# Kernel tuning notes

Measured on AMD Instinct MI355X. Metric: run time of the kernel, lower is better.

## Reference

```python
import jax, jax.numpy as jnp
import numpy as np

B, S, R, H, NH, HD = 32, 1026, 256, 1024, 16, 64

def setup_inputs() -> dict:
    key = jax.random.key(0)
    ks = jax.random.split(key, 8)
    sc = 0.02
    return {
        "q_low": jax.random.normal(ks[0], (B, S, R), jnp.float32),
        "k_low": jax.random.normal(ks[1], (B, S, R), jnp.float32),
        "v_low": jax.random.normal(ks[2], (B, S, R), jnp.float32),
        "Wq": jax.random.normal(ks[3], (R, H), jnp.float32) * sc,
        "bq": jnp.zeros((H,), jnp.float32),
        "Wk": jax.random.normal(ks[4], (R, H), jnp.float32) * sc,
        "bk": jnp.zeros((H,), jnp.float32),
        "Wv": jax.random.normal(ks[5], (R, H), jnp.float32) * sc,
        "bv": jnp.zeros((H,), jnp.float32),
        "Wo_down": jax.random.normal(ks[6], (H, R), jnp.float32) * sc,
    }

def reference(q_low, k_low, v_low, Wq, bq, Wk, bk, Wv, bv, Wo_down):
    # Up-project low-rank activations to full Q, K, V: [B,S,R] @ [R,H] -> [B,S,H]
    q = q_low @ Wq + bq
    k = k_low @ Wk + bk
    v = v_low @ Wv + bv
    # split heads: [B,S,NH,HD] -> [B,NH,S,HD]
    def split(x):
        return x.reshape(B, S, NH, HD).transpose(0, 2, 1, 3)
    qh, kh, vh = split(q), split(k), split(v)
    scores = jnp.einsum('bhqd,bhkd->bhqk', qh, kh) / jnp.sqrt(jnp.float32(HD))
    probs = jax.nn.softmax(scores, axis=-1)  # dropout p=0
    ctx = jnp.einsum('bhqk,bhkd->bhqd', probs, vh)
    ctx = ctx.transpose(0, 2, 1, 3).reshape(B, S, H)
    # Down-project with low-rank activation (gelu)
    out_low = jax.nn.gelu(ctx @ Wo_down, approximate=False)
    return out_low
```

## Files before the change

kernel.cpp:

```cpp
#include <hip/hip_runtime.h>
#include <hip/hip_bf16.h>
#include <math.h>

using short8   = __attribute__((ext_vector_type(8))) short;
using floatx4  = __attribute__((ext_vector_type(4))) float;
using floatx16 = __attribute__((ext_vector_type(16))) float;

#define B_N  32
#define S_N  1026
#define R_N  256
#define H_N  1024
#define NH_N 16
#define HD_N 64
#define SP_N 1088
#define KTILES 17

__device__ __forceinline__ float bf2f(__hip_bfloat16 x) { return __bfloat162float(x); }
__device__ __forceinline__ __hip_bfloat16 f2bf(float x) { return __float2bfloat16(x); }

__device__ __forceinline__ float fast_exp2(float x) {
#if __has_builtin(__builtin_amdgcn_exp2f)
    return __builtin_amdgcn_exp2f(x);
#else
    return exp2f(x);
#endif
}

__device__ __forceinline__ unsigned cvtpk(float lo, float hi_) {
    unsigned r;
    asm("v_cvt_pk_bf16_f32 %0, %1, %2" : "=v"(r) : "v"(lo), "v"(hi_));
    return r;
}

__device__ __forceinline__ void gl_lds16(const void* g, void* l) {
    __builtin_amdgcn_global_load_lds(
        (const __attribute__((address_space(1))) unsigned int*)g,
        (__attribute__((address_space(3))) unsigned int*)l, 16, 0, 0);
}

__device__ __forceinline__ short8 cvt8(const float* __restrict__ p) {
    floatx4 a = *(const floatx4*)p;
    floatx4 b = *(const floatx4*)(p + 4);
    short8 o;
    __hip_bfloat16* op = (__hip_bfloat16*)&o;
    op[0] = f2bf(a[0]); op[1] = f2bf(a[1]); op[2] = f2bf(a[2]); op[3] = f2bf(a[3]);
    op[4] = f2bf(b[0]); op[5] = f2bf(b[1]); op[6] = f2bf(b[2]); op[7] = f2bf(b[3]);
    return o;
}

__global__ __launch_bounds__(256) void transpose3_kernel(
    const float* __restrict__ a, const float* __restrict__ b, const float* __restrict__ c,
    __hip_bfloat16* __restrict__ oa, __hip_bfloat16* __restrict__ ob,
    __hip_bfloat16* __restrict__ oc, int K, int N) {
    __shared__ __hip_bfloat16 t[32][33];
    const float* in = (blockIdx.z == 0) ? a : (blockIdx.z == 1) ? b : c;
    __hip_bfloat16* out = (blockIdx.z == 0) ? oa : (blockIdx.z == 1) ? ob : oc;
    const int k0 = blockIdx.x * 32, n0 = blockIdx.y * 32;
    const int tx = threadIdx.x & 31, ty = threadIdx.x >> 5;
#pragma unroll
    for (int j = 0; j < 32; j += 8)
        t[ty + j][tx] = f2bf(in[(size_t)(k0 + ty + j) * N + n0 + tx]);
    __syncthreads();
#pragma unroll
    for (int j = 0; j < 32; j += 8)
        out[(size_t)(n0 + ty + j) * K + k0 + tx] = t[tx][ty + j];
}

__global__ __launch_bounds__(256) void transpose_kernel(const float* __restrict__ in,
                                                        __hip_bfloat16* __restrict__ out,
                                                        int K, int N) {
    __shared__ __hip_bfloat16 t[32][33];
    const int k0 = blockIdx.x * 32, n0 = blockIdx.y * 32;
    const int tx = threadIdx.x & 31, ty = threadIdx.x >> 5;
#pragma unroll
    for (int j = 0; j < 32; j += 8)
        t[ty + j][tx] = f2bf(in[(size_t)(k0 + ty + j) * N + n0 + tx]);
    __syncthreads();
#pragma unroll
    for (int j = 0; j < 32; j += 8)
        out[(size_t)(n0 + ty + j) * K + k0 + tx] = t[tx][ty + j];
}

__global__ __launch_bounds__(256) void cvtx_kernel(
    const float* __restrict__ q, const float* __restrict__ k, const float* __restrict__ v,
    __hip_bfloat16* __restrict__ oq, __hip_bfloat16* __restrict__ ok,
    __hip_bfloat16* __restrict__ ov, int n8) {
    int idx = blockIdx.x * 256 + threadIdx.x;
    if (idx >= n8) return;
    const float* s = (blockIdx.y == 0) ? q : (blockIdx.y == 1) ? k : v;
    __hip_bfloat16* d = (blockIdx.y == 0) ? oq : (blockIdx.y == 1) ? ok : ov;
    *(short8*)(d + (size_t)idx * 8) = cvt8(s + (size_t)idx * 8);
}

__global__ void padv_kernel(__hip_bfloat16* __restrict__ Vt, int total) {
    int idx = blockIdx.x * 256 + threadIdx.x;
    if (idx < total) {
        int p  = idx % (SP_N - S_N);
        int rd = idx / (SP_N - S_N);
        Vt[(size_t)rd * SP_N + S_N + p] = f2bf(0.f);
    }
}

__global__ __launch_bounds__(256) void qkvproj_kernel(
    const __hip_bfloat16* __restrict__ Xq, const __hip_bfloat16* __restrict__ Xk,
    const __hip_bfloat16* __restrict__ Xv,
    const __hip_bfloat16* __restrict__ WqT, const __hip_bfloat16* __restrict__ WkT,
    const __hip_bfloat16* __restrict__ WvT,
    const float* __restrict__ bq, const float* __restrict__ bk,
    const float* __restrict__ bv,
    __hip_bfloat16* __restrict__ Qc, __hip_bfloat16* __restrict__ Kc,
    __hip_bfloat16* __restrict__ Vc, int Mc, float qscale) {
    __shared__ __hip_bfloat16 As[2][128][32];
    __shared__ __hip_bfloat16 Bs[2][128][32];
    const int z = blockIdx.z;
    const __hip_bfloat16* X  = (z == 0) ? Xq  : (z == 1) ? Xk  : Xv;
    const __hip_bfloat16* WT = (z == 0) ? WqT : (z == 1) ? WkT : WvT;
    const float* bias        = (z == 0) ? bq  : (z == 1) ? bk  : bv;
    __hip_bfloat16* out      = (z == 0) ? Qc  : (z == 1) ? Kc  : Vc;
    const float oscale = (z == 0) ? qscale : 1.0f;
    const int mode = (z == 2);

    const int tid  = threadIdx.x;
    const int wave = tid >> 6, lane = tid & 63;
    const int quad = lane >> 4, l16 = lane & 15;
    const int tm = blockIdx.x * 128, tn = blockIdx.y * 128;
    const int mw = (wave >> 1) * 64, nw = (wave & 1) * 64;
    const int lrow = lane >> 2, lchunk = lane & 3;

    floatx4 acc[4][4] = {};

    const int g0 = wave, g1 = wave + 4;
    int ra0 = tm + g0 * 16 + lrow; if (ra0 >= Mc) ra0 = Mc - 1;
    int ra1 = tm + g1 * 16 + lrow; if (ra1 >= Mc) ra1 = Mc - 1;
    const int rb0 = tn + g0 * 16 + lrow, rb1 = tn + g1 * 16 + lrow;

    auto stage = [&](int bb, int kk) {
        gl_lds16(X  + (size_t)ra0 * R_N + kk + lchunk * 8, &As[bb][g0 * 16][0]);
        gl_lds16(X  + (size_t)ra1 * R_N + kk + lchunk * 8, &As[bb][g1 * 16][0]);
        gl_lds16(WT + (size_t)rb0 * R_N + kk + lchunk * 8, &Bs[bb][g0 * 16][0]);
        gl_lds16(WT + (size_t)rb1 * R_N + kk + lchunk * 8, &Bs[bb][g1 * 16][0]);
    };

    stage(0, 0);
    __syncthreads();

    for (int t = 0; t < R_N / 32; ++t) {
        const int bb = t & 1;
        if (t + 1 < R_N / 32) stage(bb ^ 1, (t + 1) * 32);
        short8 af[4], bfr[4];
#pragma unroll
        for (int mb = 0; mb < 4; ++mb) af[mb]  = *(short8*)&As[bb][mw + mb * 16 + l16][quad * 8];
#pragma unroll
        for (int nb = 0; nb < 4; ++nb) bfr[nb] = *(short8*)&Bs[bb][nw + nb * 16 + l16][quad * 8];
        if (mode == 0) {
#pragma unroll
            for (int mb = 0; mb < 4; ++mb)
#pragma unroll
                for (int nb = 0; nb < 4; ++nb)
                    acc[mb][nb] = __builtin_amdgcn_mfma_f32_16x16x32_bf16(af[mb], bfr[nb], acc[mb][nb], 0, 0, 0);
        } else {
#pragma unroll
            for (int mb = 0; mb < 4; ++mb)
#pragma unroll
                for (int nb = 0; nb < 4; ++nb)
                    acc[mb][nb] = __builtin_amdgcn_mfma_f32_16x16x32_bf16(bfr[nb], af[mb], acc[mb][nb], 0, 0, 0);
        }
        __syncthreads();
    }

#pragma unroll
    for (int mb = 0; mb < 4; ++mb)
#pragma unroll
        for (int nb = 0; nb < 4; ++nb)
#pragma unroll
            for (int r = 0; r < 4; ++r) {
                int m, n;
                if (mode == 0) { m = tm + mw + mb * 16 + quad * 4 + r; n = tn + nw + nb * 16 + l16; }
                else           { n = tn + nw + nb * 16 + quad * 4 + r; m = tm + mw + mb * 16 + l16; }
                if (m >= Mc) continue;
                float v = oscale * (acc[mb][nb][r] + bias[n]);
                int bl = m / S_N, s = m - bl * S_N;
                int h = n >> 6, d = n & 63;
                size_t off = (mode == 0)
                    ? ((size_t)((bl * NH_N + h) * S_N + s)) * HD_N + d
                    : ((size_t)((bl * NH_N + h) * HD_N + d)) * SP_N + s;
                out[off] = f2bf(v);
            }
}

__global__ __launch_bounds__(256, 3) void attn_kernel(
    const __hip_bfloat16* __restrict__ Qh,
    const __hip_bfloat16* __restrict__ Kh,
    const __hip_bfloat16* __restrict__ Vt,
    __hip_bfloat16* __restrict__ ctx) {
    __shared__ __hip_bfloat16 Kl[2][64][64];
    __shared__ __hip_bfloat16 Vl[2][64][64];

    const int bh  = blockIdx.x;
    const int q0  = blockIdx.y * 128;
    const int tid = threadIdx.x;
    const int wave = tid >> 6, lane = tid & 63;
    const int c = lane & 31, hi = lane >> 5, c7 = c & 7;
    const size_t base  = (size_t)bh * S_N * HD_N;
    const size_t vbase = (size_t)bh * HD_N * SP_N;

    const int lr = lane >> 3;
    const int sc = (lane & 7) ^ lr;

    short8 qf[4];
    {
        int qrow = q0 + wave * 32 + c;
        if (qrow > S_N - 1) qrow = S_N - 1;
        const __hip_bfloat16* qp = Qh + base + (size_t)qrow * HD_N + hi * 8;
#pragma unroll
        for (int i = 0; i < 4; ++i) qf[i] = *(const short8*)(qp + 16 * i);
    }

    floatx16 oacc[2] = {};
    float lsum = 0.f;

    auto stage = [&](int bb, int kt) {
#pragma unroll
        for (int j = 0; j < 2; ++j) {
            int r = 16 * wave + 8 * j + lr;
            int krow = kt + r;
            if (krow > S_N - 1) krow = S_N - 1;
            gl_lds16(Kh + base + (size_t)krow * HD_N + sc * 8,
                     &Kl[bb][16 * wave + 8 * j][0]);
            gl_lds16(Vt + vbase + (size_t)r * SP_N + kt + sc * 8,
                     &Vl[bb][16 * wave + 8 * j][0]);
        }
    };

    stage(0, 0);
    __syncthreads();

    int bb = 0;
    for (int t = 0; t < KTILES; ++t) {
        const int kt = t * 64;
        if (t + 1 < KTILES) stage(bb ^ 1, kt + 64);
        const bool last = (kt + 64 > S_N);

        short8 pa[2][2];
#pragma unroll
        for (int sub = 0; sub < 2; ++sub) {
            floatx16 sacc = {};
            __builtin_amdgcn_s_setprio(1);
#pragma unroll
            for (int i = 0; i < 4; ++i) {
                short8 kf = *(const short8*)&Kl[bb][32 * sub + c][(((2 * i + hi) ^ c7) << 3)];
                sacc = __builtin_amdgcn_mfma_f32_32x32x16_bf16(kf, qf[i], sacc, 0, 0, 0);
            }
            __builtin_amdgcn_s_setprio(0);
            float ps[16];
            if (!last) {
#pragma unroll
                for (int r = 0; r < 16; ++r) ps[r] = fast_exp2(sacc[r]);
            } else {
#pragma unroll
                for (int r = 0; r < 16; ++r) {
                    int key = kt + 32 * sub + (r & 3) + 8 * (r >> 2) + 4 * hi;
                    ps[r] = (key < S_N) ? fast_exp2(sacc[r]) : 0.f;
                }
            }
#pragma unroll
            for (int r = 0; r < 16; ++r) lsum += ps[r];
#pragma unroll
            for (int step = 0; step < 2; ++step) {
                unsigned w0 = cvtpk(ps[8 * step + 0], ps[8 * step + 1]);
                unsigned w1 = cvtpk(ps[8 * step + 2], ps[8 * step + 3]);
                unsigned w2 = cvtpk(ps[8 * step + 4], ps[8 * step + 5]);
                unsigned w3 = cvtpk(ps[8 * step + 6], ps[8 * step + 7]);
                asm("v_permlane32_swap_b32 %0, %1" : "+v"(w0), "+v"(w2));
                asm("v_permlane32_swap_b32 %0, %1" : "+v"(w1), "+v"(w3));
                union { unsigned u[4]; short8 s; } fu;
                fu.u[0] = w0; fu.u[1] = w1; fu.u[2] = w2; fu.u[3] = w3;
                pa[sub][step] = fu.s;
            }
        }

        __builtin_amdgcn_s_setprio(1);
#pragma unroll
        for (int db = 0; db < 2; ++db)
#pragma unroll
            for (int sub = 0; sub < 2; ++sub)
#pragma unroll
                for (int step = 0; step < 2; ++step) {
                    short8 vf = *(const short8*)
                        &Vl[bb][32 * db + c][((((sub * 2 + step) * 2 + hi) ^ c7) << 3)];
                    oacc[db] = __builtin_amdgcn_mfma_f32_32x32x16_bf16(pa[sub][step], vf, oacc[db], 0, 0, 0);
                }
        __builtin_amdgcn_s_setprio(0);

        __syncthreads();
        bb ^= 1;
    }

    lsum += __shfl_xor(lsum, 32);
    float rs = 1.0f / lsum;

    const int bl = bh / NH_N, h = bh - bl * NH_N;
    const int srow0 = q0 + wave * 32;
#pragma unroll
    for (int r = 0; r < 16; ++r) {
        int q = (r & 3) + 8 * (r >> 2) + 4 * hi;
        float rr = __shfl(rs, q, 32);
        int s = srow0 + q;
        if (s < S_N) {
            size_t o = ((size_t)(bl * S_N + s)) * H_N + h * HD_N + c;
            ctx[o]      = f2bf(oacc[0][r] * rr);
            ctx[o + 32] = f2bf(oacc[1][r] * rr);
        }
    }
}

__global__ __launch_bounds__(256) void dproj_kernel(
    const __hip_bfloat16* __restrict__ X,
    const __hip_bfloat16* __restrict__ WT,
    float* __restrict__ out,
    int Mc) {
    __shared__ __hip_bfloat16 As[2][128][32];
    __shared__ __hip_bfloat16 Bs[2][128][32];
    const int tid  = threadIdx.x;
    const int wave = tid >> 6, lane = tid & 63;
    const int quad = lane >> 4, l16 = lane & 15;
    const int tm = blockIdx.x * 128, tn = blockIdx.y * 128;
    const int mw = (wave >> 1) * 64, nw = (wave & 1) * 64;
    const int lrow = lane >> 2, lchunk = lane & 3;

    floatx4 acc[4][4] = {};

    const int g0 = wave, g1 = wave + 4;
    int ra0 = tm + g0 * 16 + lrow; if (ra0 >= Mc) ra0 = Mc - 1;
    int ra1 = tm + g1 * 16 + lrow; if (ra1 >= Mc) ra1 = Mc - 1;
    const int rb0 = tn + g0 * 16 + lrow, rb1 = tn + g1 * 16 + lrow;

    auto stage = [&](int bb, int kk) {
        gl_lds16(X  + (size_t)ra0 * H_N + kk + lchunk * 8, &As[bb][g0 * 16][0]);
        gl_lds16(X  + (size_t)ra1 * H_N + kk + lchunk * 8, &As[bb][g1 * 16][0]);
        gl_lds16(WT + (size_t)rb0 * H_N + kk + lchunk * 8, &Bs[bb][g0 * 16][0]);
        gl_lds16(WT + (size_t)rb1 * H_N + kk + lchunk * 8, &Bs[bb][g1 * 16][0]);
    };

    stage(0, 0);
    __syncthreads();

    for (int t = 0; t < H_N / 32; ++t) {
        const int bb = t & 1;
        if (t + 1 < H_N / 32) stage(bb ^ 1, (t + 1) * 32);
        short8 af[4], bfr[4];
#pragma unroll
        for (int mb = 0; mb < 4; ++mb) af[mb]  = *(short8*)&As[bb][mw + mb * 16 + l16][quad * 8];
#pragma unroll
        for (int nb = 0; nb < 4; ++nb) bfr[nb] = *(short8*)&Bs[bb][nw + nb * 16 + l16][quad * 8];
#pragma unroll
        for (int mb = 0; mb < 4; ++mb)
#pragma unroll
            for (int nb = 0; nb < 4; ++nb)
                acc[mb][nb] = __builtin_amdgcn_mfma_f32_16x16x32_bf16(af[mb], bfr[nb], acc[mb][nb], 0, 0, 0);
        __syncthreads();
    }

#pragma unroll
    for (int mb = 0; mb < 4; ++mb)
#pragma unroll
        for (int nb = 0; nb < 4; ++nb)
#pragma unroll
            for (int r = 0; r < 4; ++r) {
                int m = tm + mw + mb * 16 + quad * 4 + r;
                int n = tn + nw + nb * 16 + l16;
                if (m >= Mc) continue;
                float x = acc[mb][nb][r];
                float g = 0.5f * x * (1.0f + erff(x * 0.70710678118654752f));
                out[(size_t)m * R_N + n] = g;
            }
}

extern "C" void kernel_launch(void* const* d_in, const int* in_sizes, int n_in,
                              void* d_out, int out_size, void* d_ws, size_t ws_size,
                              hipStream_t stream) {
    const float* q_low = (const float*)d_in[0];
    const float* k_low = (const float*)d_in[1];
    const float* v_low = (const float*)d_in[2];
    const float* Wq    = (const float*)d_in[3];
    const float* bq    = (const float*)d_in[4];
    const float* Wk    = (const float*)d_in[5];
    const float* bk    = (const float*)d_in[6];
    const float* Wv    = (const float*)d_in[7];
    const float* bv    = (const float*)d_in[8];
    const float* Wo    = (const float*)d_in[9];
    float* out = (float*)d_out;
    (void)in_sizes; (void)n_in; (void)out_size;

    const float QSCALE = 0.125f * 1.44269504088896f;
    const size_t SZ_W = (size_t)H_N * R_N * 2;

    int C = 32;
    while (C > 1) {
        size_t qk = (size_t)C * NH_N * S_N * HD_N * 2;
        size_t vv = (size_t)C * NH_N * HD_N * SP_N * 2;
        size_t cx = (size_t)C * S_N * H_N * 2;
        if (4 * SZ_W + 2 * qk + vv + cx <= ws_size) break;
        C >>= 1;
    }

    char* ws = (char*)d_ws;
    const size_t SZ_QK = (size_t)C * NH_N * S_N * HD_N * 2;
    const size_t SZ_V  = (size_t)C * NH_N * HD_N * SP_N * 2;
    __hip_bfloat16* WqT = (__hip_bfloat16*)(ws);
    __hip_bfloat16* WkT = (__hip_bfloat16*)(ws + SZ_W);
    __hip_bfloat16* WvT = (__hip_bfloat16*)(ws + 2 * SZ_W);
    __hip_bfloat16* WoT = (__hip_bfloat16*)(ws + 3 * SZ_W);
    __hip_bfloat16* Qc  = (__hip_bfloat16*)(ws + 4 * SZ_W);
    __hip_bfloat16* Kc  = (__hip_bfloat16*)(ws + 4 * SZ_W + SZ_QK);
    __hip_bfloat16* Vc  = (__hip_bfloat16*)(ws + 4 * SZ_W + 2 * SZ_QK);
    __hip_bfloat16* ctc = (__hip_bfloat16*)(ws + 4 * SZ_W + 2 * SZ_QK + SZ_V);

    {
        dim3 tg(R_N / 32, H_N / 32, 3);
        transpose3_kernel<<<tg, 256, 0, stream>>>(Wq, Wk, Wv, WqT, WkT, WvT, R_N, H_N);
        dim3 to(H_N / 32, R_N / 32);
        transpose_kernel<<<to, 256, 0, stream>>>(Wo, WoT, H_N, R_N);
    }

    {
        int total = C * NH_N * HD_N * (SP_N - S_N);
        padv_kernel<<<(total + 255) / 256, 256, 0, stream>>>(Vc, total);
    }

    for (int c0 = 0; c0 < B_N; c0 += C) {
        const int Mc = C * S_N;
        const size_t xoff = (size_t)c0 * S_N * R_N;

        __hip_bfloat16* Xq = ctc;
        __hip_bfloat16* Xk = ctc + (size_t)Mc * R_N;
        __hip_bfloat16* Xv = ctc + 2 * (size_t)Mc * R_N;
        {
            int n8 = Mc * R_N / 8;
            dim3 cg((n8 + 255) / 256, 3);
            cvtx_kernel<<<cg, 256, 0, stream>>>(q_low + xoff, k_low + xoff, v_low + xoff,
                                                Xq, Xk, Xv, n8);
        }

        dim3 pg((Mc + 127) / 128, H_N / 128, 3);
        qkvproj_kernel<<<pg, 256, 0, stream>>>(Xq, Xk, Xv, WqT, WkT, WvT,
                                               bq, bk, bv, Qc, Kc, Vc, Mc, QSCALE);

        dim3 ag(C * NH_N, (S_N + 127) / 128);
        attn_kernel<<<ag, 256, 0, stream>>>(Qc, Kc, Vc, ctc);

        dim3 dg((Mc + 127) / 128, R_N / 128);
        dproj_kernel<<<dg, 256, 0, stream>>>(ctc, WoT, out + xoff, Mc);
    }
}
```

Measured before the change: 643.4 us.

## Widen GEMM K-tiles with swizzled LDS, XCD-remap blocks, shrink dproj M-tile

```diff
diff --git a/kernel.cpp b/kernel.cpp
--- a/kernel.cpp
+++ b/kernel.cpp
@@ -36,6 +36,10 @@
     __builtin_amdgcn_global_load_lds(
         (const __attribute__((address_space(1))) unsigned int*)g,
         (__attribute__((address_space(3))) unsigned int*)l, 16, 0, 0);
+}
+
+__device__ __forceinline__ int xcd_swz(int o, int nwg) {
+    return ((nwg & 7) == 0) ? ((o & 7) * (nwg >> 3) + (o >> 3)) : o;
 }
 
 __device__ __forceinline__ short8 cvt8(const float* __restrict__ p) {
@@ -110,60 +114,83 @@
     const float* __restrict__ bv,
     __hip_bfloat16* __restrict__ Qc, __hip_bfloat16* __restrict__ Kc,
     __hip_bfloat16* __restrict__ Vc, int Mc, float qscale) {
-    __shared__ __hip_bfloat16 As[2][128][32];
-    __shared__ __hip_bfloat16 Bs[2][128][32];
-    const int z = blockIdx.z;
-    const __hip_bfloat16* X  = (z == 0) ? Xq  : (z == 1) ? Xk  : Xv;
-    const __hip_bfloat16* WT = (z == 0) ? WqT : (z == 1) ? WkT : WvT;
-    const float* bias        = (z == 0) ? bq  : (z == 1) ? bk  : bv;
-    __hip_bfloat16* out      = (z == 0) ? Qc  : (z == 1) ? Kc  : Vc;
-    const float oscale = (z == 0) ? qscale : 1.0f;
-    const int mode = (z == 2);
+    __shared__ __hip_bfloat16 As[2][128][64];
+    __shared__ __hip_bfloat16 Bs[2][128][64];
+
+    const int nx = gridDim.x;
+    const int nwg = nx * 8 * 3;
+    const int o = blockIdx.x + nx * (blockIdx.y + 8 * blockIdx.z);
+    const int tlin = xcd_swz(o, nwg);
+    const int ty = tlin & 7;
+    const int rest = tlin >> 3;
+    const int tx = rest % nx, tz = rest / nx;
+
+    const __hip_bfloat16* X  = (tz == 0) ? Xq  : (tz == 1) ? Xk  : Xv;
+    const __hip_bfloat16* WT = (tz == 0) ? WqT : (tz == 1) ? WkT : WvT;
+    const float* bias        = (tz == 0) ? bq  : (tz == 1) ? bk  : bv;
+    __hip_bfloat16* out      = (tz == 0) ? Qc  : (tz == 1) ? Kc  : Vc;
+    const float oscale = (tz == 0) ? qscale : 1.0f;
+    const int mode = (tz == 2);
 
     const int tid  = threadIdx.x;
     const int wave = tid >> 6, lane = tid & 63;
     const int quad = lane >> 4, l16 = lane & 15;
-    const int tm = blockIdx.x * 128, tn = blockIdx.y * 128;
+    const int tm = tx * 128, tn = ty * 128;
     const int mw = (wave >> 1) * 64, nw = (wave & 1) * 64;
-    const int lrow = lane >> 2, lchunk = lane & 3;
+    const int lr = lane >> 3;
+    const int sc = (lane & 7) ^ lr;
 
     floatx4 acc[4][4] = {};
 
-    const int g0 = wave, g1 = wave + 4;
-    int ra0 = tm + g0 * 16 + lrow; if (ra0 >= Mc) ra0 = Mc - 1;
-    int ra1 = tm + g1 * 16 + lrow; if (ra1 >= Mc) ra1 = Mc - 1;
-    const int rb0 = tn + g0 * 16 + lrow, rb1 = tn + g1 * 16 + lrow;
-
     auto stage = [&](int bb, int kk) {
-        gl_lds16(X  + (size_t)ra0 * R_N + kk + lchunk * 8, &As[bb][g0 * 16][0]);
-        gl_lds16(X  + (size_t)ra1 * R_N + kk + lchunk * 8, &As[bb][g1 * 16][0]);
-        gl_lds16(WT + (size_t)rb0 * R_N + kk + lchunk * 8, &Bs[bb][g0 * 16][0]);
-        gl_lds16(WT + (size_t)rb1 * R_N + kk + lchunk * 8, &Bs[bb][g1 * 16][0]);
+#pragma unroll
+        for (int s8 = 0; s8 < 4; ++s8) {
+            int row = wave * 32 + s8 * 8;
+            int gm = tm + row + lr; if (gm >= Mc) gm = Mc - 1;
+            gl_lds16(X + (size_t)gm * R_N + kk + sc * 8, &As[bb][row][0]);
+            gl_lds16(WT + (size_t)(tn + row + lr) * R_N + kk + sc * 8, &Bs[bb][row][0]);
+        }
     };
 
     stage(0, 0);
     __syncthreads();
 
-    for (int t = 0; t < R_N / 32; ++t) {
+    for (int t = 0; t < R_N / 64; ++t) {
         const int bb = t & 1;
-        if (t + 1 < R_N / 32) stage(bb ^ 1, (t + 1) * 32);
-        short8 af[4], bfr[4];
-#pragma unroll
-        for (int mb = 0; mb < 4; ++mb) af[mb]  = *(short8*)&As[bb][mw + mb * 16 + l16][quad * 8];
-#pragma unroll
-        for (int nb = 0; nb < 4; ++nb) bfr[nb] = *(short8*)&Bs[bb][nw + nb * 16 + l16][quad * 8];
+        if (t + 1 < R_N / 64) stage(bb ^ 1, (t + 1) * 64);
+        short8 af[4][2], bfr[4][2];
+#pragma unroll
+        for (int mb = 0; mb < 4; ++mb) {
+            int row = mw + mb * 16 + l16;
+            const char* rp = (const char*)&As[bb][row][0];
+#pragma unroll
+            for (int k2 = 0; k2 < 2; ++k2)
+                af[mb][k2] = *(const short8*)(rp + ((((k2 * 4 + quad)) ^ (row & 7)) << 4));
+        }
+#pragma unroll
+        for (int nb = 0; nb < 4; ++nb) {
+            int row = nw + nb * 16 + l16;
+            const char* rp = (const char*)&Bs[bb][row][0];
+#pragma unroll
+            for (int k2 = 0; k2 < 2; ++k2)
+                bfr[nb][k2] = *(const short8*)(rp + ((((k2 * 4 + quad)) ^ (row & 7)) << 4));
+        }
         if (mode == 0) {
 #pragma unroll
             for (int mb = 0; mb < 4; ++mb)
 #pragma unroll
-                for (int nb = 0; nb < 4; ++nb)
-                    acc[mb][nb] = __builtin_amdgcn_mfma_f32_16x16x32_bf16(af[mb], bfr[nb], acc[mb][nb], 0, 0, 0);
+                for (int nb = 0; nb < 4; ++nb) {
+                    acc[mb][nb] = __builtin_amdgcn_mfma_f32_16x16x32_bf16(af[mb][0], bfr[nb][0], acc[mb][nb], 0, 0, 0);
+                    acc[mb][nb] = __builtin_amdgcn_mfma_f32_16x16x32_bf16(af[mb][1], bfr[nb][1], acc[mb][nb], 0, 0, 0);
+                }
         } else {
 #pragma unroll
             for (int mb = 0; mb < 4; ++mb)
 #pragma unroll
-                for (int nb = 0; nb < 4; ++nb)
-                    acc[mb][nb] = __builtin_amdgcn_mfma_f32_16x16x32_bf16(bfr[nb], af[mb], acc[mb][nb], 0, 0, 0);
+                for (int nb = 0; nb < 4; ++nb) {
+                    acc[mb][nb] = __builtin_amdgcn_mfma_f32_16x16x32_bf16(bfr[nb][0], af[mb][0], acc[mb][nb], 0, 0, 0);
+                    acc[mb][nb] = __builtin_amdgcn_mfma_f32_16x16x32_bf16(bfr[nb][1], af[mb][1], acc[mb][nb], 0, 0, 0);
+                }
         }
         __syncthreads();
     }
@@ -196,8 +223,13 @@
     __shared__ __hip_bfloat16 Kl[2][64][64];
     __shared__ __hip_bfloat16 Vl[2][64][64];
 
-    const int bh  = blockIdx.x;
-    const int q0  = blockIdx.y * 128;
+    const int ny = gridDim.y;
+    const int nwg = gridDim.x * ny;
+    const int o = blockIdx.x + gridDim.x * blockIdx.y;
+    const int tlin = xcd_swz(o, nwg);
+    const int bh = tlin / ny;
+    const int q0 = (tlin % ny) * 128;
+
     const int tid = threadIdx.x;
     const int wave = tid >> 6, lane = tid & 63;
     const int c = lane & 31, hi = lane >> 5, c7 = c & 7;
@@ -307,9 +339,9 @@
         float rr = __shfl(rs, q, 32);
         int s = srow0 + q;
         if (s < S_N) {
-            size_t o = ((size_t)(bl * S_N + s)) * H_N + h * HD_N + c;
-            ctx[o]      = f2bf(oacc[0][r] * rr);
-            ctx[o + 32] = f2bf(oacc[1][r] * rr);
+            size_t o2 = ((size_t)(bl * S_N + s)) * H_N + h * HD_N + c;
+            ctx[o2]      = f2bf(oacc[0][r] * rr);
+            ctx[o2 + 32] = f2bf(oacc[1][r] * rr);
         }
     }
 }
@@ -319,50 +351,70 @@
     const __hip_bfloat16* __restrict__ WT,
     float* __restrict__ out,
     int Mc) {
-    __shared__ __hip_bfloat16 As[2][128][32];
-    __shared__ __hip_bfloat16 Bs[2][128][32];
+    __shared__ __hip_bfloat16 As[2][64][64];
+    __shared__ __hip_bfloat16 Bs[2][128][64];
+
+    const int tx = blockIdx.x, ty = blockIdx.y;
+
     const int tid  = threadIdx.x;
     const int wave = tid >> 6, lane = tid & 63;
     const int quad = lane >> 4, l16 = lane & 15;
-    const int tm = blockIdx.x * 128, tn = blockIdx.y * 128;
-    const int mw = (wave >> 1) * 64, nw = (wave & 1) * 64;
-    const int lrow = lane >> 2, lchunk = lane & 3;
-
-    floatx4 acc[4][4] = {};
-
-    const int g0 = wave, g1 = wave + 4;
-    int ra0 = tm + g0 * 16 + lrow; if (ra0 >= Mc) ra0 = Mc - 1;
-    int ra1 = tm + g1 * 16 + lrow; if (ra1 >= Mc) ra1 = Mc - 1;
-    const int rb0 = tn + g0 * 16 + lrow, rb1 = tn + g1 * 16 + lrow;
+    const int tm = tx * 64, tn = ty * 128;
+    const int mw = (wave >> 1) * 32, nw = (wave & 1) * 64;
+    const int lr = lane >> 3;
+    const int sc = (lane & 7) ^ lr;
+
+    floatx4 acc[2][4] = {};
 
     auto stage = [&](int bb, int kk) {
-        gl_lds16(X  + (size_t)ra0 * H_N + kk + lchunk * 8, &As[bb][g0 * 16][0]);
-        gl_lds16(X  + (size_t)ra1 * H_N + kk + lchunk * 8, &As[bb][g1 * 16][0]);
-        gl_lds16(WT + (size_t)rb0 * H_N + kk + lchunk * 8, &Bs[bb][g0 * 16][0]);
-        gl_lds16(WT + (size_t)rb1 * H_N + kk + lchunk * 8, &Bs[bb][g1 * 16][0]);
+#pragma unroll
+        for (int s8 = 0; s8 < 2; ++s8) {
+            int row = wave * 16 + s8 * 8;
+            int gm = tm + row + lr; if (gm >= Mc) gm = Mc - 1;
+            gl_lds16(X + (size_t)gm * H_N + kk + sc * 8, &As[bb][row][0]);
+        }
+#pragma unroll
+        for (int s8 = 0; s8 < 4; ++s8) {
+            int row = wave * 32 + s8 * 8;
+            gl_lds16(WT + (size_t)(tn + row + lr) * H_N + kk + sc * 8, &Bs[bb][row][0]);
+        }
     };
 
     stage(0, 0);
     __syncthreads();
 
-    for (int t = 0; t < H_N / 32; ++t) {
+    for (int t = 0; t < H_N / 64; ++t) {
         const int bb = t & 1;
-        if (t + 1 < H_N / 32) stage(bb ^ 1, (t + 1) * 32);
-        short8 af[4], bfr[4];
-#pragma unroll
-        for (int mb = 0; mb < 4; ++mb) af[mb]  = *(short8*)&As[bb][mw + mb * 16 + l16][quad * 8];
-#pragma unroll
-        for (int nb = 0; nb < 4; ++nb) bfr[nb] = *(short8*)&Bs[bb][nw + nb * 16 + l16][quad * 8];
-#pragma unroll
-        for (int mb = 0; mb < 4; ++mb)
-#pragma unroll
-            for (int nb = 0; nb < 4; ++nb)
-                acc[mb][nb] = __builtin_amdgcn_mfma_f32_16x16x32_bf16(af[mb], bfr[nb], acc[mb][nb], 0, 0, 0);
+        if (t + 1 < H_N / 64) stage(bb ^ 1, (t + 1) * 64);
+        short8 af[2][2], bfr[4][2];
+#pragma unroll
+        for (int mb = 0; mb < 2; ++mb) {
+            int row = mw + mb * 16 + l16;
+            const char* rp = (const char*)&As[bb][row][0];
+#pragma unroll
+            for (int k2 = 0; k2 < 2; ++k2)
+                af[mb][k2] = *(const short8*)(rp + ((((k2 * 4 + quad)) ^ (row & 7)) << 4));
+        }
+#pragma unroll
+        for (int nb = 0; nb < 4; ++nb) {
+            int row = nw + nb * 16 + l16;
+            const char* rp = (const char*)&Bs[bb][row][0];
+#pragma unroll
+            for (int k2 = 0; k2 < 2; ++k2)
+                bfr[nb][k2] = *(const short8*)(rp + ((((k2 * 4 + quad)) ^ (row & 7)) << 4));
+        }
+#pragma unroll
+        for (int mb = 0; mb < 2; ++mb)
+#pragma unroll
+            for (int nb = 0; nb < 4; ++nb) {
+                acc[mb][nb] = __builtin_amdgcn_mfma_f32_16x16x32_bf16(af[mb][0], bfr[nb][0], acc[mb][nb], 0, 0, 0);
+                acc[mb][nb] = __builtin_amdgcn_mfma_f32_16x16x32_bf16(af[mb][1], bfr[nb][1], acc[mb][nb], 0, 0, 0);
+            }
         __syncthreads();
     }
 
 #pragma unroll
-    for (int mb = 0; mb < 4; ++mb)
+    for (int mb = 0; mb < 2; ++mb)
 #pragma unroll
         for (int nb = 0; nb < 4; ++nb)
 #pragma unroll
@@ -449,7 +501,7 @@
         dim3 ag(C * NH_N, (S_N + 127) / 128);
         attn_kernel<<<ag, 256, 0, stream>>>(Qc, Kc, Vc, ctc);
 
-        dim3 dg((Mc + 127) / 128, R_N / 128);
+        dim3 dg((Mc + 63) / 64, R_N / 128);
         dproj_kernel<<<dg, 256, 0, stream>>>(ctc, WoT, out + xoff, Mc);
     }
 }
```

New measurement: 559.7 us. 13.0% less time.
